# Kernel tuning notes

Hardware: AMD Instinct MI355X
Metric: run time of the kernel (lower is better)

Reference implementation:

```python
import jax, jax.numpy as jnp
import numpy as np

EPS = 1e-9
LDIM = 4  # dim_g + dim_t + dim_b + dim_w


def _mvn_logpdf(v, F):
    # batched zero-mean multivariate normal log-density, v: (N,O), F: (N,O,O)
    chol = jnp.linalg.cholesky(F)
    z = jax.scipy.linalg.solve_triangular(chol, v[..., None], lower=True)[..., 0]
    quad = jnp.sum(z * z, axis=-1)
    logdet = 2.0 * jnp.sum(jnp.log(jnp.diagonal(chol, axis1=-2, axis2=-1)), axis=-1)
    k = v.shape[-1]
    return -0.5 * (quad + logdet + k * jnp.log(2.0 * jnp.pi))


def _forward(y, B_G, B_T, B_B, B_W, lambda_r1_free, lambda_r2_free,
             q_diag, r_diag, gamma1, gamma2_learnable):
    N, Nt, O = y.shape
    L = LDIM
    # ----- _build_matrices -----
    B11 = jnp.zeros((L, L)).at[0, 0].set(B_G[0, 0]).at[1, 1].set(B_T[0, 0]).at[2, 2].set(B_B[0, 0])
    B22 = jnp.zeros((L, L)).at[3, 3].set(B_W[0, 0])
    B12 = jnp.zeros((L, L)).at[3, :3].set(1.0 / 3.0)  # regime1 factors feed shared factor
    B21 = jnp.zeros((L, L))
    L1 = jnp.zeros((O, L))
    L1 = L1.at[0, 0].set(1.0).at[1, 0].set(lambda_r1_free[0]).at[2, 0].set(lambda_r1_free[1])
    L1 = L1.at[3, 1].set(1.0).at[4, 1].set(lambda_r1_free[2]).at[5, 1].set(lambda_r1_free[3])
    L1 = L1.at[6, 2].set(1.0).at[7, 2].set(lambda_r1_free[4]).at[8, 2].set(lambda_r1_free[5])
    L2 = jnp.zeros((O, L)).at[0, 3].set(1.0).at[1:, 3].set(lambda_r2_free)
    Q = jnp.diag(jnp.abs(q_diag) + 1e-4)
    R = jnp.diag(jnp.abs(r_diag) + 1e-4)
    F_JIT = 1e-5 * jnp.eye(O)
    I_L = jnp.eye(L)
    P22_CONST = 0.9999

    # ----- initial beliefs ('informative') -----
    prob0 = jnp.tile(jnp.array([0.99, 0.01], jnp.float32), (N, 1))
    eta0 = jnp.zeros((N, L), y.dtype)
    P0 = jnp.tile(jnp.diag(jnp.array([1000.0, 1000.0, 1000.0, 1e-9], y.dtype))[None], (N, 1, 1))

    def predict(B, eta, P):
        # eta: (N,L), P: (N,L,L)
        return eta @ B.T, jnp.einsum('ij,njk,lk->nil', B, P, B) + Q

    def innov(Lm, e, Pp, y_t):
        v = y_t - e @ Lm.T
        F = jnp.einsum('oi,nij,pj->nop', Lm, Pp, Lm) + R + F_JIT
        return v, F

    def kupdate(e, Pp, Lm, v, F):
        LP = jnp.einsum('oi,nij->noj', Lm, Pp)          # (N,O,L)
        K = jnp.swapaxes(jnp.linalg.solve(F, LP), -1, -2)  # P Lm^T F^{-1}, (N,L,O)
        e_u = e + jnp.einsum('nlo,no->nl', K, v)
        IKL = I_L - K @ Lm                                # (N,L,L)
        P_u = IKL @ Pp @ jnp.swapaxes(IKL, -1, -2) + jnp.einsum('nlo,op,nmp->nlm', K, R, K)
        return e_u, P_u

    def collapse(w_a, w_b, e_a, e_b, P_a, P_b):
        e = w_a[:, None] * e_a + w_b[:, None] * e_b
        da, db = e_a - e, e_b - e
        P = (w_a[:, None, None] * (P_a + da[:, :, None] * da[:, None, :])
             + w_b[:, None, None] * (P_b + db[:, :, None] * db[:, None, :]))
        return e, P

    def step(carry, y_t):
        prob, eta1, eta2, P1, P2, ll = carry
        # HMM transition: p11 depends on regime-1 state (first L-1 components)
        logit_p11 = gamma1 + eta1[:, :3] @ gamma2_learnable
        p11 = jax.nn.sigmoid(logit_p11)
        # predictions for the 4 regime transitions (origin -> destination)
        e11, Pp11 = predict(B11, eta1, P1)
        e12, Pp12 = predict(B21, eta2, P2)
        e21, Pp21 = predict(B12, eta1, P1)
        e22, Pp22 = predict(B22, eta2, P2)
        v11, F11 = innov(L1, e11, Pp11, y_t)
        v12, F12 = innov(L1, e12, Pp12, y_t)
        v21, F21 = innov(L2, e21, Pp21, y_t)
        v22, F22 = innov(L2, e22, Pp22, y_t)
        ll11 = _mvn_logpdf(v11, F11)
        ll12 = _mvn_logpdf(v12, F12)
        ll21 = _mvn_logpdf(v21, F21)
        ll22 = _mvn_logpdf(v22, F22)
        lp = jnp.log(prob + EPS)
        c11 = lp[:, 0] + jnp.log(p11 + EPS) + ll11
        c12 = lp[:, 1] + np.log(1.0 - P22_CONST + EPS) + ll12
        c21 = lp[:, 0] + jnp.log(1.0 - p11 + EPS) + ll21
        c22 = lp[:, 1] + np.log(P22_CONST + EPS) + ll22
        logp = jnp.stack([c11, c12, c21, c22], axis=1)
        ll_t = jax.scipy.special.logsumexp(logp, axis=1)
        pt = jnp.exp(logp - ll_t[:, None])
        pr1 = pt[:, 0] + pt[:, 1]
        pr2 = pt[:, 2] + pt[:, 3]
        W11 = pt[:, 0] / (pr1 + EPS)
        W12 = pt[:, 1] / (pr1 + EPS)
        W21 = pt[:, 2] / (pr2 + EPS)
        W22 = pt[:, 3] / (pr2 + EPS)
        eu11, Pu11 = kupdate(e11, Pp11, L1, v11, F11)
        eu12, Pu12 = kupdate(e12, Pp12, L1, v12, F12)
        eu21, Pu21 = kupdate(e21, Pp21, L2, v21, F21)
        eu22, Pu22 = kupdate(e22, Pp22, L2, v22, F22)
        eta1n, P1n = collapse(W11, W12, eu11, eu12, Pu11, Pu12)
        eta2n, P2n = collapse(W21, W22, eu21, eu22, Pu21, Pu22)
        probn = jnp.stack([pr1, pr2], axis=1)
        return (probn, eta1n, eta2n, P1n, P2n, ll + ll_t.sum()), None

    carry0 = (prob0, eta0, eta0, P0, P0, jnp.zeros((), y.dtype))
    (_, _, _, _, _, total_ll), _ = jax.lax.scan(step, carry0, jnp.swapaxes(y, 0, 1))
    return total_ll


def setup_inputs() -> dict:
    key = jax.random.key(0)
    ks = jax.random.split(key, 12)
    N, Nt, O = 16384, 64, 9
    f32 = jnp.float32
    return {
        'y': jax.random.normal(ks[0], (N, Nt, O), f32),
        'B_G': jax.random.uniform(ks[1], (1, 1), f32, 0.6, 0.95),  # Beta(5,1.5)-like AR coeffs
        'B_T': jax.random.uniform(ks[2], (1, 1), f32, 0.6, 0.95),
        'B_B': jax.random.uniform(ks[3], (1, 1), f32, 0.6, 0.95),
        'B_W': jax.random.uniform(ks[4], (1, 1), f32, 0.6, 0.95),
        'lambda_r1_free': jax.random.normal(ks[5], (6,), f32),
        'lambda_r2_free': jax.random.normal(ks[6], (O - 1,), f32),
        'q_diag': jax.random.uniform(ks[7], (LDIM,), f32),
        'r_diag': jax.random.uniform(ks[8], (O,), f32),
        'gamma1': jnp.abs(jax.random.normal(ks[9], (), f32)),
        'gamma2_learnable': jax.random.normal(ks[10], (LDIM - 1,), f32),
    }


def reference(y, B_G, B_T, B_B, B_W, lambda_r1_free, lambda_r2_free,
              q_diag, r_diag, gamma1, gamma2_learnable):
    return _forward(y, B_G, B_T, B_B, B_W, lambda_r1_free, lambda_r2_free,
                    q_diag, r_diag, gamma1, gamma2_learnable)
```

## Files before the change

kernel.cpp:

```cpp
#include <hip/hip_runtime.h>


typedef float v2f __attribute__((ext_vector_type(2)));

static __device__ __forceinline__ float frcp(float x)  { return __builtin_amdgcn_rcpf(x); }
static __device__ __forceinline__ float frsq(float x)  { return __builtin_amdgcn_rsqf(x); }
static __device__ __forceinline__ float fexp2(float x) { return __builtin_amdgcn_exp2f(x); }
static __device__ __forceinline__ float flog2(float x) { return __builtin_amdgcn_logf(x); }
static __device__ __forceinline__ v2f   splat(float s) { return (v2f){s, s}; }

#define EPSF   1e-9f
#define L2E    1.4426950408889634f
#define LN2    0.6931471805599453f
#define L2_2PI_9 23.86346461225016f
#define C12F   1.00001e-4f
#define P22F   0.99990001f
#define QK     (-0.5f * L2E)

__global__ __launch_bounds__(64, 1)
void kf_kernel(const float* __restrict__ y,
               const float* __restrict__ pBG, const float* __restrict__ pBT,
               const float* __restrict__ pBB, const float* __restrict__ pBW,
               const float* __restrict__ lam1, const float* __restrict__ lam2,
               const float* __restrict__ qd,  const float* __restrict__ rd,
               const float* __restrict__ pG1, const float* __restrict__ pG2,
               float* __restrict__ partial, int N, int Nt)
{
    const int lane = threadIdx.x;
    const int n = blockIdx.x * 64 + lane;
    const bool valid = (n < N);
    const int rowlen = Nt * 9;
    const int nchunk = Nt / 4;

    const float bg = pBG[0], bt = pBT[0], bb = pBB[0], bw = pBW[0];
    float a[9], l2v[9], id[9], ld[9];
    a[0] = 1.f; a[1] = lam1[0]; a[2] = lam1[1];
    a[3] = 1.f; a[4] = lam1[2]; a[5] = lam1[3];
    a[6] = 1.f; a[7] = lam1[4]; a[8] = lam1[5];
    l2v[0] = 1.f;
    #pragma unroll
    for (int i = 0; i < 8; ++i) l2v[i + 1] = lam2[i];
    float l2detD = 0.f;
    #pragma unroll
    for (int o = 0; o < 9; ++o) {
        float dv = fabsf(rd[o]) + 1.0e-4f + 1.0e-5f;
        id[o] = 1.0f / dv;
        ld[o] = l2v[o] * id[o];
        l2detD += flog2(dv);
    }
    const float q0 = fabsf(qd[0]) + 1e-4f, q1 = fabsf(qd[1]) + 1e-4f;
    const float q2 = fabsf(qd[2]) + 1e-4f, q3 = fabsf(qd[3]) + 1e-4f;
    const float g0 = a[0]*a[0]*id[0] + a[1]*a[1]*id[1] + a[2]*a[2]*id[2];
    const float g1 = a[3]*a[3]*id[3] + a[4]*a[4]*id[4] + a[5]*a[5]*id[5];
    const float g2 = a[6]*a[6]*id[6] + a[7]*a[7]*id[7] + a[8]*a[8]*id[8];
    float h = 0.f;
    #pragma unroll
    for (int o = 0; o < 9; ++o) h += l2v[o] * ld[o];
    const float pk0 = q0 / (1.f + q0 * g0);
    const float pk1 = q1 / (1.f + q1 * g1);
    const float pk2 = q2 / (1.f + q2 * g2);
    const float C12D = C12F * frsq((1.f + q0*g0) * (1.f + q1*g1) * (1.f + q2*g2));
    const float gam1 = pG1[0], w0 = pG2[0], w1 = pG2[1], w2 = pG2[2];
    const float CC = -0.5f * (l2detD + L2_2PI_9);

    const v2f av01 = {a[0], a[1]}, av23 = {a[2], a[3]}, av45 = {a[4], a[5]}, av67 = {a[6], a[7]};
    const float a8 = a[8];
    const v2f idv01 = {id[0], id[1]}, idv23 = {id[2], id[3]}, idv45 = {id[4], id[5]}, idv67 = {id[6], id[7]};
    const float id8 = id[8];
    const v2f ldv01 = {ld[0], ld[1]}, ldv23 = {ld[2], ld[3]}, ldv45 = {ld[4], ld[5]}, ldv67 = {ld[6], ld[7]};
    const float ld8 = ld[8];
    const v2f cS0 = {bg*bg, bg*bt}, cS1 = {bg*bb, bt*bt}, cS2 = {bt*bb, bb*bb};
    const v2f qS0 = {q0, 0.f},  qS1 = {0.f, q1},  qS2 = {0.f, q2};
    const v2f pkv0 = {pk0, 0.f}, pkv1 = {0.f, pk1}, pkv2 = {0.f, pk2};
    const v2f bgt = {bg, bt};

    float pf1 = 0.99f + EPSF, pf2 = 0.01f + EPSF;
    v2f se01 = {0.f, 0.f};  float se2 = 0.f;
    v2f Pv0 = {1000.f, 0.f};
    v2f Pv1 = {0.f, 1000.f};
    v2f Pv2 = {0.f, 1000.f};
    float sm2 = 0.f, sp2 = 1e-9f;
    float acc2 = 0.0f;

    const float* row = y + (size_t)(valid ? n : 0) * rowlen;

    float4 A[9], B[9];
    #pragma unroll
    for (int i = 0; i < 9; ++i) A[i] = *(const float4*)(row + i * 4);

    auto step4 = [&](const float4 (&buf)[9]) {
        #pragma unroll
        for (int s = 0; s < 4; ++s) {
            float yv[9];
            #pragma unroll
            for (int o = 0; o < 9; ++o) {
                const int idx = s * 9 + o, vno = idx >> 2, cm = idx & 3;
                yv[o] = (cm == 0) ? buf[vno].x : (cm == 1) ? buf[vno].y
                      : (cm == 2) ? buf[vno].z : buf[vno].w;
            }
            const v2f yvv0 = {yv[0], yv[1]}, yvv1 = {yv[2], yv[3]};
            const v2f yvv2 = {yv[4], yv[5]}, yvv3 = {yv[6], yv[7]};
            const float yv8 = yv[8];

            const float se0 = se01.x, se1 = se01.y;
            float logit = gam1 + w0 * se0 + w1 * se1 + w2 * se2;
            float esig = fexp2(-logit * L2E);
            float p11 = frcp(1.f + esig);
            float pf11 = p11 + EPSF;
            float pf21 = 1.f - p11 + EPSF;

            v2f ep01 = bgt * se01;
            float ep0 = ep01.x, ep1 = ep01.y, ep2 = bb * se2;
            v2f Sv0 = cS0 * Pv0 + qS0;
            v2f Sv1 = cS1 * Pv1 + qS1;
            v2f Sv2 = cS2 * Pv2 + qS2;
            float S00 = Sv0.x, S01 = Sv0.y, S02 = Sv1.x;
            float S11 = Sv1.y, S12 = Sv2.x, S22 = Sv2.y;

            v2f vv0 = yvv0 - av01 * splat(ep0);
            v2f vv1 = yvv1 - av23 * ep01;
            v2f vv2 = yvv2 - av45 * splat(ep1);
            v2f vv3 = yvv3 - av67 * splat(ep2);
            float v8 = yv8 - a8 * ep2;
            v2f w0v = idv01 * vv0, w1v = idv23 * vv1, w2v = idv45 * vv2, w3v = idv67 * vv3;
            float w8 = id8 * v8;
            v2f pA = av01 * w0v, pB = av23 * w1v, pC = av45 * w2v, pD = av67 * w3v;
            float u0 = pA.x + pA.y + pB.x;
            float u1 = pB.y + pC.x + pC.y;
            float u2 = pD.x + pD.y + a8 * w8;
            v2f vds = vv0 * w0v + vv1 * w1v + vv2 * w2v + vv3 * w3v;
            float vdv = vds.x + vds.y + v8 * w8;
            v2f ylv = ldv01 * yvv0 + ldv23 * yvv1 + ldv45 * yvv2 + ldv67 * yvv3;
            float yl = ylv.x + ylv.y + ld8 * yv8;

            float M00 = S00*g0 + 1.f, M01 = S01*g1,       M02 = S02*g2;
            float M10 = S01*g0,       M11 = S11*g1 + 1.f, M12 = S12*g2;
            float M20 = S02*g0,       M21 = S12*g1,       M22 = S22*g2 + 1.f;
            float adj00 = M11*M22 - M12*M21, adj01 = M02*M21 - M01*M22, adj02 = M01*M12 - M02*M11;
            float adj10 = M12*M20 - M10*M22, adj11 = M00*M22 - M02*M20, adj12 = M02*M10 - M00*M12;
            float adj20 = M10*M21 - M11*M20, adj21 = M01*M20 - M00*M21, adj22 = M00*M11 - M01*M10;
            float detM = M00*adj00 + M01*adj10 + M02*adj20;
            float iM = frcp(detM);
            float N00 = adj00*S00 + adj01*S01 + adj02*S02;
            float N01 = adj00*S01 + adj01*S11 + adj02*S12;
            float N02 = adj00*S02 + adj01*S12 + adj02*S22;
            float N11 = adj10*S01 + adj11*S11 + adj12*S12;
            float N12 = adj10*S02 + adj11*S12 + adj12*S22;
            float N22 = adj20*S02 + adj21*S12 + adj22*S22;
            v2f Civ0 = (v2f){N00, N01} * splat(iM);
            v2f Civ1 = (v2f){N02, N11} * splat(iM);
            v2f Civ2 = (v2f){N12, N22} * splat(iM);
            float Ci00 = Civ0.x, Ci01 = Civ0.y, Ci02 = Civ1.x;
            float Ci11 = Civ1.y, Ci12 = Civ2.x, Ci22 = Civ2.y;
            float t0 = Ci00*u0 + Ci01*u1 + Ci02*u2;
            float t1 = Ci01*u0 + Ci11*u1 + Ci12*u2;
            float t2 = Ci02*u0 + Ci12*u1 + Ci22*u2;
            float quad11 = vdv - (u0*t0 + u1*t1 + u2*t2);
            v2f euv01 = ep01 + (v2f){t0, t1};
            float eu2 = ep2 + t2;

            float u120 = u0 + g0*ep0, u121 = u1 + g1*ep1, u122 = u2 + g2*ep2;
            float ydy = vdv + 2.f*(ep0*u0 + ep1*u1 + ep2*u2)
                      + g0*ep0*ep0 + g1*ep1*ep1 + g2*ep2*ep2;
            float quad12 = ydy - (pk0*u120*u120 + pk1*u121*u121 + pk2*u122*u122);
            v2f f01 = (v2f){pk0*u120, pk1*u121};
            float f2 = pk2*u122;

            float m21 = (se0 + se1 + se2) * (1.0f / 3.0f);
            float sP = Pv0.x + Pv1.y + Pv2.y + 2.f*(Pv0.y + Pv1.x + Pv2.x);
            v2f m2v = {m21, bw * sm2};
            v2f pv  = {q3 + sP * (1.0f / 9.0f), bw*bw*sp2 + q3};
            v2f u1v = splat(yl) - m2v * splat(h);
            v2f vdav = splat(ydy) - m2v * (splat(2.f * yl) - m2v * splat(h));
            v2f denv = splat(1.f) + pv * splat(h);
            v2f idev = {frcp(denv.x), frcp(denv.y)};
            v2f puv = pv * idev;
            v2f quadv = vdav - puv * u1v * u1v;
            v2f euv = m2v + puv * u1v;

            float q11e = QK * quad11, q12e = QK * quad12;
            v2f  q2v  = splat(QK) * quadv;
            float Mq = fmaxf(fmaxf(q11e, q12e), fmaxf(q2v.x, q2v.y));
            float w11 = pf1 * pf11 * frsq(detM) * fexp2(q11e - Mq);
            float w12 = pf2 * C12D * fexp2(q12e - Mq);
            float w21 = pf1 * pf21 * frsq(denv.x) * fexp2(q2v.x - Mq);
            float w22 = pf2 * P22F * frsq(denv.y) * fexp2(q2v.y - Mq);
            float ssum = w11 + w12 + w21 + w22;
            acc2 += Mq + flog2(ssum);
            float pr1n = w11 + w12, pr2n = w21 + w22;
            float den1 = pr1n + EPSF * ssum;
            float den2 = pr2n + EPSF * ssum;
            float inv1 = frcp(den1), inv2 = frcp(den2);
            float W11 = w11 * inv1, W12 = w12 * inv1;
            float W21 = w21 * inv2, W22 = w22 * inv2;
            float issum = frcp(ssum);
            pf1 = pr1n * issum + EPSF;
            pf2 = pr2n * issum + EPSF;

            v2f nev01 = splat(W11) * euv01 + splat(W12) * f01;
            float ne2 = W11 * eu2 + W12 * f2;
            v2f dav01 = euv01 - nev01;  float da2 = eu2 - ne2;
            v2f dbv01 = f01 - nev01;    float db2 = f2 - ne2;
            float da0 = dav01.x, da1 = dav01.y, db0 = dbv01.x, db1 = dbv01.y;
            Pv0 = splat(W11) * (Civ0 + splat(da0) * dav01)
                + splat(W12) * (pkv0 + splat(db0) * dbv01);
            Pv1 = splat(W11) * (Civ1 + dav01 * (v2f){da2, da1})
                + splat(W12) * (pkv1 + dbv01 * (v2f){db2, db1});
            Pv2 = splat(W11) * (Civ2 + (v2f){da1, da2} * splat(da2))
                + splat(W12) * (pkv2 + (v2f){db1, db2} * splat(db2));
            se01 = nev01; se2 = ne2;

            float nm2 = W21 * euv.x + W22 * euv.y;
            float dc = euv.x - nm2, dd = euv.y - nm2;
            sp2 = W21 * (puv.x + dc*dc) + W22 * (puv.y + dd*dd);
            sm2 = nm2;
        }
    };

    for (int c = 0; c < nchunk; c += 2) {
        if (c + 1 < nchunk) {
            const float* p = row + (c + 1) * 36;
            #pragma unroll
            for (int i = 0; i < 9; ++i) B[i] = *(const float4*)(p + i * 4);
        }
        step4(A);
        if (c + 2 < nchunk) {
            const float* p = row + (c + 2) * 36;
            #pragma unroll
            for (int i = 0; i < 9; ++i) A[i] = *(const float4*)(p + i * 4);
        }
        step4(B);
    }

    float acc = valid ? (acc2 + (float)Nt * CC) * LN2 : 0.0f;
    #pragma unroll
    for (int off = 32; off; off >>= 1) acc += __shfl_down(acc, off, 64);
    if (lane == 0) partial[blockIdx.x] = acc;
}

__global__ __launch_bounds__(64)
void reduce_k(const float* __restrict__ part, float* __restrict__ out, int nb)
{
    float s = 0.f;
    for (int i = threadIdx.x; i < nb; i += 64) s += part[i];
    #pragma unroll
    for (int off = 32; off; off >>= 1) s += __shfl_down(s, off, 64);
    if (threadIdx.x == 0) out[0] = s;
}

extern "C" void kernel_launch(void* const* d_in, const int* in_sizes, int n_in,
                              void* d_out, int out_size, void* d_ws, size_t ws_size,
                              hipStream_t stream)
{
    const float* y    = (const float*)d_in[0];
    const float* pBG  = (const float*)d_in[1];
    const float* pBT  = (const float*)d_in[2];
    const float* pBB  = (const float*)d_in[3];
    const float* pBW  = (const float*)d_in[4];
    const float* lam1 = (const float*)d_in[5];
    const float* lam2 = (const float*)d_in[6];
    const float* qd   = (const float*)d_in[7];
    const float* rd   = (const float*)d_in[8];
    const float* pG1  = (const float*)d_in[9];
    const float* pG2  = (const float*)d_in[10];

    const int total = in_sizes[0];
    const int Nt = 64, O = 9;
    const int N = total / (Nt * O);
    const int blocks = (N + 63) / 64;

    float* partial = (float*)d_ws;
    kf_kernel<<<blocks, 64, 0, stream>>>(y, pBG, pBT, pBB, pBW, lam1, lam2,
                                         qd, rd, pG1, pG2, partial, N, Nt);
    reduce_k<<<1, 64, 0, stream>>>(partial, (float*)d_out, blocks);
}
```

Baseline: 127.4 us.

## Split each series across a quad of lanes with DPP exchanges

Each time series is now handled by 4 lanes instead of one. Three of them own one block of the 3x3 regime-1 factor state and the fourth is idle padding. Cross-lane terms such as sums, the 3x3 cofactors and the covariance update are exchanged with DPP quad rotations and xor-reductions. This launches four times as many waves, which is meant to raise occupancy and cut the serial per-lane work on a latency-bound recurrence. The cost is a wasted lane in every quad, redundant scalar regime-2 math in every lane, narrower scalar loads in place of float4, and rsq squared used in place of rcp for the inverse determinant.

```diff
diff --git a/kernel.cpp b/kernel.cpp
--- a/kernel.cpp
+++ b/kernel.cpp
@@ -7,7 +7,23 @@
 static __device__ __forceinline__ float frsq(float x)  { return __builtin_amdgcn_rsqf(x); }
 static __device__ __forceinline__ float fexp2(float x) { return __builtin_amdgcn_exp2f(x); }
 static __device__ __forceinline__ float flog2(float x) { return __builtin_amdgcn_logf(x); }
-static __device__ __forceinline__ v2f   splat(float s) { return (v2f){s, s}; }
+
+template <int CTRL>
+static __device__ __forceinline__ float dppf(float x) {
+    int i = __float_as_int(x);
+    i = __builtin_amdgcn_mov_dpp(i, CTRL, 0xF, 0xF, true);
+    return __int_as_float(i);
+}
+#define ROTL 0xC9
+#define ROTR 0xD2
+#define XOR1 0xB1
+#define XOR2 0x4E
+
+static __device__ __forceinline__ float qsum(float x) {
+    x += dppf<XOR1>(x);
+    x += dppf<XOR2>(x);
+    return x;
+}
 
 #define EPSF   1e-9f
 #define L2E    1.4426950408889634f
@@ -27,8 +43,11 @@
                float* __restrict__ partial, int N, int Nt)
 {
     const int lane = threadIdx.x;
-    const int n = blockIdx.x * 64 + lane;
-    const bool valid = (n < N);
+    const int j    = lane & 3;
+    const int sid  = (blockIdx.x * 64 + lane) >> 2;
+    const bool valid = (sid < N);
+    const bool isRow = (j < 3);
+    const int jj = isRow ? j : 0;
     const int rowlen = Nt * 9;
     const int nchunk = Nt / 4;
 
@@ -60,179 +79,145 @@
     const float pk1 = q1 / (1.f + q1 * g1);
     const float pk2 = q2 / (1.f + q2 * g2);
     const float C12D = C12F * frsq((1.f + q0*g0) * (1.f + q1*g1) * (1.f + q2*g2));
-    const float gam1 = pG1[0], w0 = pG2[0], w1 = pG2[1], w2 = pG2[2];
+    const float gam1 = pG1[0], w0c = pG2[0], w1c = pG2[1], w2c = pG2[2];
     const float CC = -0.5f * (l2detD + L2_2PI_9);
 
-    const v2f av01 = {a[0], a[1]}, av23 = {a[2], a[3]}, av45 = {a[4], a[5]}, av67 = {a[6], a[7]};
-    const float a8 = a[8];
-    const v2f idv01 = {id[0], id[1]}, idv23 = {id[2], id[3]}, idv45 = {id[4], id[5]}, idv67 = {id[6], id[7]};
-    const float id8 = id[8];
-    const v2f ldv01 = {ld[0], ld[1]}, ldv23 = {ld[2], ld[3]}, ldv45 = {ld[4], ld[5]}, ldv67 = {ld[6], ld[7]};
-    const float ld8 = ld[8];
-    const v2f cS0 = {bg*bg, bg*bt}, cS1 = {bg*bb, bt*bt}, cS2 = {bt*bb, bb*bb};
-    const v2f qS0 = {q0, 0.f},  qS1 = {0.f, q1},  qS2 = {0.f, q2};
-    const v2f pkv0 = {pk0, 0.f}, pkv1 = {0.f, pk1}, pkv2 = {0.f, pk2};
-    const v2f bgt = {bg, bt};
+    auto sel3 = [&](float x0, float x1, float x2) {
+        float r = (jj == 1) ? x1 : x0;
+        return (jj == 2) ? x2 : r;
+    };
+    const float aO0 = sel3(a[0], a[3], a[6]), aO1 = sel3(a[1], a[4], a[7]), aO2 = sel3(a[2], a[5], a[8]);
+    const float iO0 = sel3(id[0], id[3], id[6]), iO1 = sel3(id[1], id[4], id[7]), iO2 = sel3(id[2], id[5], id[8]);
+    const float lO0 = sel3(ld[0], ld[3], ld[6]), lO1 = sel3(ld[1], ld[4], ld[7]), lO2 = sel3(ld[2], ld[5], ld[8]);
+    const float bS = sel3(bg, bt, bb), bN = sel3(bt, bb, bg), bP = sel3(bb, bg, bt);
+    const float gS = sel3(g0, g1, g2), gN = sel3(g1, g2, g0), gP = sel3(g2, g0, g1);
+    const float qS = sel3(q0, q1, q2);
+    const float pkS = sel3(pk0, pk1, pk2);
+    const float wS = sel3(w0c, w1c, w2c);
+
+    auto z3 = [&](float x) { return isRow ? x : 0.0f; };
 
     float pf1 = 0.99f + EPSF, pf2 = 0.01f + EPSF;
-    v2f se01 = {0.f, 0.f};  float se2 = 0.f;
-    v2f Pv0 = {1000.f, 0.f};
-    v2f Pv1 = {0.f, 1000.f};
-    v2f Pv2 = {0.f, 1000.f};
+    float seJ = 0.f;
+    float Pr0 = 1000.f, Pr1 = 0.f, Pr2 = 0.f;
     float sm2 = 0.f, sp2 = 1e-9f;
     float acc2 = 0.0f;
 
-    const float* row = y + (size_t)(valid ? n : 0) * rowlen;
-
-    float4 A[9], B[9];
-    #pragma unroll
-    for (int i = 0; i < 9; ++i) A[i] = *(const float4*)(row + i * 4);
-
-    auto step4 = [&](const float4 (&buf)[9]) {
+    const float* row = y + (size_t)(valid ? sid : 0) * rowlen + 3 * jj;
+    float A[12], B[12];
+    auto loadChunk = [&](float (&buf)[12], int c) {
+        const float* p = row + c * 36;
         #pragma unroll
         for (int s = 0; s < 4; ++s) {
-            float yv[9];
-            #pragma unroll
-            for (int o = 0; o < 9; ++o) {
-                const int idx = s * 9 + o, vno = idx >> 2, cm = idx & 3;
-                yv[o] = (cm == 0) ? buf[vno].x : (cm == 1) ? buf[vno].y
-                      : (cm == 2) ? buf[vno].z : buf[vno].w;
-            }
-            const v2f yvv0 = {yv[0], yv[1]}, yvv1 = {yv[2], yv[3]};
-            const v2f yvv2 = {yv[4], yv[5]}, yvv3 = {yv[6], yv[7]};
-            const float yv8 = yv[8];
-
-            const float se0 = se01.x, se1 = se01.y;
-            float logit = gam1 + w0 * se0 + w1 * se1 + w2 * se2;
+            buf[s*3+0] = p[s*9+0];
+            buf[s*3+1] = p[s*9+1];
+            buf[s*3+2] = p[s*9+2];
+        }
+    };
+    loadChunk(A, 0);
+
+    auto step4 = [&](const float (&buf)[12]) {
+        #pragma unroll
+        for (int s = 0; s < 4; ++s) {
+            const float y0 = buf[s*3+0], y1 = buf[s*3+1], y2 = buf[s*3+2];
+
+            float logit = gam1 + qsum(z3(wS * seJ));
             float esig = fexp2(-logit * L2E);
             float p11 = frcp(1.f + esig);
-            float pf11 = p11 + EPSF;
-            float pf21 = 1.f - p11 + EPSF;
-
-            v2f ep01 = bgt * se01;
-            float ep0 = ep01.x, ep1 = ep01.y, ep2 = bb * se2;
-            v2f Sv0 = cS0 * Pv0 + qS0;
-            v2f Sv1 = cS1 * Pv1 + qS1;
-            v2f Sv2 = cS2 * Pv2 + qS2;
-            float S00 = Sv0.x, S01 = Sv0.y, S02 = Sv1.x;
-            float S11 = Sv1.y, S12 = Sv2.x, S22 = Sv2.y;
-
-            v2f vv0 = yvv0 - av01 * splat(ep0);
-            v2f vv1 = yvv1 - av23 * ep01;
-            v2f vv2 = yvv2 - av45 * splat(ep1);
-            v2f vv3 = yvv3 - av67 * splat(ep2);
-            float v8 = yv8 - a8 * ep2;
-            v2f w0v = idv01 * vv0, w1v = idv23 * vv1, w2v = idv45 * vv2, w3v = idv67 * vv3;
-            float w8 = id8 * v8;
-            v2f pA = av01 * w0v, pB = av23 * w1v, pC = av45 * w2v, pD = av67 * w3v;
-            float u0 = pA.x + pA.y + pB.x;
-            float u1 = pB.y + pC.x + pC.y;
-            float u2 = pD.x + pD.y + a8 * w8;
-            v2f vds = vv0 * w0v + vv1 * w1v + vv2 * w2v + vv3 * w3v;
-            float vdv = vds.x + vds.y + v8 * w8;
-            v2f ylv = ldv01 * yvv0 + ldv23 * yvv1 + ldv45 * yvv2 + ldv67 * yvv3;
-            float yl = ylv.x + ylv.y + ld8 * yv8;
-
-            float M00 = S00*g0 + 1.f, M01 = S01*g1,       M02 = S02*g2;
-            float M10 = S01*g0,       M11 = S11*g1 + 1.f, M12 = S12*g2;
-            float M20 = S02*g0,       M21 = S12*g1,       M22 = S22*g2 + 1.f;
-            float adj00 = M11*M22 - M12*M21, adj01 = M02*M21 - M01*M22, adj02 = M01*M12 - M02*M11;
-            float adj10 = M12*M20 - M10*M22, adj11 = M00*M22 - M02*M20, adj12 = M02*M10 - M00*M12;
-            float adj20 = M10*M21 - M11*M20, adj21 = M01*M20 - M00*M21, adj22 = M00*M11 - M01*M10;
-            float detM = M00*adj00 + M01*adj10 + M02*adj20;
-            float iM = frcp(detM);
-            float N00 = adj00*S00 + adj01*S01 + adj02*S02;
-            float N01 = adj00*S01 + adj01*S11 + adj02*S12;
-            float N02 = adj00*S02 + adj01*S12 + adj02*S22;
-            float N11 = adj10*S01 + adj11*S11 + adj12*S12;
-            float N12 = adj10*S02 + adj11*S12 + adj12*S22;
-            float N22 = adj20*S02 + adj21*S12 + adj22*S22;
-            v2f Civ0 = (v2f){N00, N01} * splat(iM);
-            v2f Civ1 = (v2f){N02, N11} * splat(iM);
-            v2f Civ2 = (v2f){N12, N22} * splat(iM);
-            float Ci00 = Civ0.x, Ci01 = Civ0.y, Ci02 = Civ1.x;
-            float Ci11 = Civ1.y, Ci12 = Civ2.x, Ci22 = Civ2.y;
-            float t0 = Ci00*u0 + Ci01*u1 + Ci02*u2;
-            float t1 = Ci01*u0 + Ci11*u1 + Ci12*u2;
-            float t2 = Ci02*u0 + Ci12*u1 + Ci22*u2;
-            float quad11 = vdv - (u0*t0 + u1*t1 + u2*t2);
-            v2f euv01 = ep01 + (v2f){t0, t1};
-            float eu2 = ep2 + t2;
-
-            float u120 = u0 + g0*ep0, u121 = u1 + g1*ep1, u122 = u2 + g2*ep2;
-            float ydy = vdv + 2.f*(ep0*u0 + ep1*u1 + ep2*u2)
-                      + g0*ep0*ep0 + g1*ep1*ep1 + g2*ep2*ep2;
-            float quad12 = ydy - (pk0*u120*u120 + pk1*u121*u121 + pk2*u122*u122);
-            v2f f01 = (v2f){pk0*u120, pk1*u121};
-            float f2 = pk2*u122;
-
-            float m21 = (se0 + se1 + se2) * (1.0f / 3.0f);
-            float sP = Pv0.x + Pv1.y + Pv2.y + 2.f*(Pv0.y + Pv1.x + Pv2.x);
-            v2f m2v = {m21, bw * sm2};
-            v2f pv  = {q3 + sP * (1.0f / 9.0f), bw*bw*sp2 + q3};
-            v2f u1v = splat(yl) - m2v * splat(h);
-            v2f vdav = splat(ydy) - m2v * (splat(2.f * yl) - m2v * splat(h));
-            v2f denv = splat(1.f) + pv * splat(h);
-            v2f idev = {frcp(denv.x), frcp(denv.y)};
-            v2f puv = pv * idev;
+            float pf11 = p11 + EPSF, pf21 = 1.f - p11 + EPSF;
+
+            float epJ = bS * seJ;
+            float S0 = bS*bS*Pr0 + qS;
+            float S1 = bS*bN*Pr1;
+            float S2 = bS*bP*Pr2;
+            float M0 = S0*gS + 1.f;
+            float M1 = S1*gN;
+            float M2 = S2*gP;
+
+            float v0 = y0 - aO0*epJ, v1 = y1 - aO1*epJ, v2 = y2 - aO2*epJ;
+            float w0v = iO0*v0, w1v = iO1*v1, w2v = iO2*v2;
+            float uJ = aO0*w0v + aO1*w1v + aO2*w2v;
+            float vdv = qsum(z3(v0*w0v + v1*w1v + v2*w2v));
+            float yl  = qsum(z3(lO0*y0 + lO1*y1 + lO2*y2));
+            float ydy = vdv + qsum(z3(epJ * (2.f*uJ + gS*epJ)));
+
+            float Mn0 = dppf<ROTL>(M0), Mn1 = dppf<ROTL>(M1), Mn2 = dppf<ROTL>(M2);
+            float Mp0 = dppf<ROTR>(M0), Mp1 = dppf<ROTR>(M1), Mp2 = dppf<ROTR>(M2);
+            float cf0 = Mn0*Mp0 - Mn1*Mp2;
+            float cf1 = Mn1*Mp1 - Mn2*Mp0;
+            float cf2 = Mn2*Mp2 - Mn0*Mp1;
+            float det = M0*cf0 + M1*cf1 + M2*cf2;
+            float rs  = frsq(det);
+            float iM  = rs * rs;
+            float cn0 = dppf<ROTL>(cf0), cn1 = dppf<ROTL>(cf1), cn2 = dppf<ROTL>(cf2);
+            float cp0 = dppf<ROTR>(cf0), cp1 = dppf<ROTR>(cf1), cp2 = dppf<ROTR>(cf2);
+            float Ci0 = iM * (S0*cf0 + S1*cn2 + S2*cp1);
+            float Ci1 = iM * (S0*cf1 + S1*cn0 + S2*cp2);
+            float Ci2 = iM * (S0*cf2 + S1*cn1 + S2*cp0);
+
+            float uN = dppf<ROTL>(uJ), uP = dppf<ROTR>(uJ);
+            float tJ = Ci0*uJ + Ci1*uN + Ci2*uP;
+            float quad11 = vdv - qsum(z3(uJ * tJ));
+            float euJ = epJ + tJ;
+
+            float u12 = uJ + gS * epJ;
+            float fJ  = pkS * u12;
+            float quad12 = ydy - qsum(z3(pkS * u12 * u12));
+
+            float seS = qsum(z3(seJ));
+            float sP  = qsum(z3(Pr0 + Pr1 + Pr2));
+            v2f m2v; m2v.x = seS * (1.f/3.f);       m2v.y = bw * sm2;
+            v2f pvv; pvv.x = q3 + sP * (1.f/9.f);   pvv.y = bw*bw*sp2 + q3;
+            v2f u1v  = (v2f){yl, yl} - m2v * (v2f){h, h};
+            v2f vdav = (v2f){ydy, ydy} - m2v * ((v2f){2.f*yl, 2.f*yl} - m2v * (v2f){h, h});
+            v2f denv = (v2f){1.f, 1.f} + pvv * (v2f){h, h};
+            v2f rvv; rvv.x = frsq(denv.x); rvv.y = frsq(denv.y);
+            v2f idev = rvv * rvv;
+            v2f puv = pvv * idev;
             v2f quadv = vdav - puv * u1v * u1v;
             v2f euv = m2v + puv * u1v;
 
             float q11e = QK * quad11, q12e = QK * quad12;
-            v2f  q2v  = splat(QK) * quadv;
-            float Mq = fmaxf(fmaxf(q11e, q12e), fmaxf(q2v.x, q2v.y));
-            float w11 = pf1 * pf11 * frsq(detM) * fexp2(q11e - Mq);
-            float w12 = pf2 * C12D * fexp2(q12e - Mq);
-            float w21 = pf1 * pf21 * frsq(denv.x) * fexp2(q2v.x - Mq);
-            float w22 = pf2 * P22F * frsq(denv.y) * fexp2(q2v.y - Mq);
+            float q21e = QK * quadv.x, q22e = QK * quadv.y;
+            float Mq = fmaxf(fmaxf(q11e, q12e), fmaxf(q21e, q22e));
+            float w11 = pf1 * pf11 * rs    * fexp2(q11e - Mq);
+            float w12 = pf2 * C12D         * fexp2(q12e - Mq);
+            float w21 = pf1 * pf21 * rvv.x * fexp2(q21e - Mq);
+            float w22 = pf2 * P22F * rvv.y * fexp2(q22e - Mq);
             float ssum = w11 + w12 + w21 + w22;
             acc2 += Mq + flog2(ssum);
             float pr1n = w11 + w12, pr2n = w21 + w22;
-            float den1 = pr1n + EPSF * ssum;
-            float den2 = pr2n + EPSF * ssum;
-            float inv1 = frcp(den1), inv2 = frcp(den2);
-            float W11 = w11 * inv1, W12 = w12 * inv1;
-            float W21 = w21 * inv2, W22 = w22 * inv2;
-            float issum = frcp(ssum);
+            float den1 = pr1n + EPSF * ssum, den2 = pr2n + EPSF * ssum;
+            float inv1 = frcp(den1), inv2 = frcp(den2), issum = frcp(ssum);
+            float W11 = w11*inv1, W12 = w12*inv1;
+            float W21 = w21*inv2, W22 = w22*inv2;
             pf1 = pr1n * issum + EPSF;
             pf2 = pr2n * issum + EPSF;
 
-            v2f nev01 = splat(W11) * euv01 + splat(W12) * f01;
-            float ne2 = W11 * eu2 + W12 * f2;
-            v2f dav01 = euv01 - nev01;  float da2 = eu2 - ne2;
-            v2f dbv01 = f01 - nev01;    float db2 = f2 - ne2;
-            float da0 = dav01.x, da1 = dav01.y, db0 = dbv01.x, db1 = dbv01.y;
-            Pv0 = splat(W11) * (Civ0 + splat(da0) * dav01)
-                + splat(W12) * (pkv0 + splat(db0) * dbv01);
-            Pv1 = splat(W11) * (Civ1 + dav01 * (v2f){da2, da1})
-                + splat(W12) * (pkv1 + dbv01 * (v2f){db2, db1});
-            Pv2 = splat(W11) * (Civ2 + (v2f){da1, da2} * splat(da2))
-                + splat(W12) * (pkv2 + (v2f){db1, db2} * splat(db2));
-            se01 = nev01; se2 = ne2;
-
-            float nm2 = W21 * euv.x + W22 * euv.y;
+            float neJ = W11*euJ + W12*fJ;
+            float daJ = euJ - neJ, dbJ = fJ - neJ;
+            float daN = dppf<ROTL>(daJ), daP = dppf<ROTR>(daJ);
+            float dbN = dppf<ROTL>(dbJ), dbP = dppf<ROTR>(dbJ);
+            Pr0 = W11*(Ci0 + daJ*daJ) + W12*(pkS + dbJ*dbJ);
+            Pr1 = W11*(Ci1 + daJ*daN) + W12*(dbJ*dbN);
+            Pr2 = W11*(Ci2 + daJ*daP) + W12*(dbJ*dbP);
+            seJ = neJ;
+
+            float nm2 = W21*euv.x + W22*euv.y;
             float dc = euv.x - nm2, dd = euv.y - nm2;
-            sp2 = W21 * (puv.x + dc*dc) + W22 * (puv.y + dd*dd);
+            sp2 = W21*(puv.x + dc*dc) + W22*(puv.y + dd*dd);
             sm2 = nm2;
         }
     };
 
     for (int c = 0; c < nchunk; c += 2) {
-        if (c + 1 < nchunk) {
-            const float* p = row + (c + 1) * 36;
-            #pragma unroll
-            for (int i = 0; i < 9; ++i) B[i] = *(const float4*)(p + i * 4);
-        }
+        if (c + 1 < nchunk) loadChunk(B, c + 1);
         step4(A);
-        if (c + 2 < nchunk) {
-            const float* p = row + (c + 2) * 36;
-            #pragma unroll
-            for (int i = 0; i < 9; ++i) A[i] = *(const float4*)(p + i * 4);
-        }
+        if (c + 2 < nchunk) loadChunk(A, c + 2);
         step4(B);
     }
 
-    float acc = valid ? (acc2 + (float)Nt * CC) * LN2 : 0.0f;
+    float acc = (valid && j == 0) ? (acc2 + (float)Nt * CC) * LN2 : 0.0f;
     #pragma unroll
     for (int off = 32; off; off >>= 1) acc += __shfl_down(acc, off, 64);
     if (lane == 0) partial[blockIdx.x] = acc;
@@ -267,7 +252,7 @@
     const int total = in_sizes[0];
     const int Nt = 64, O = 9;
     const int N = total / (Nt * O);
-    const int blocks = (N + 63) / 64;
+    const int blocks = (N * 4 + 63) / 64;
 
     float* partial = (float*)d_ws;
     kf_kernel<<<blocks, 64, 0, stream>>>(y, pBG, pBT, pBB, pBW, lam1, lam2,
```

New measurement: 126.7 us (median of 2 runs). Within noise of the previous version (-0.6%).
